# Performance work log

Measured on AMD Instinct MI355X. Metric: run time of the kernel, lower is better.

## Reference

```python
import jax, jax.numpy as jnp
import numpy as np

VOCAB = 32000
EMB = 1024
HID = 1024
CHUNK = 64
NCH = HID // CHUNK          # 16 master-gate chunks
G = 4 * HID + 2 * NCH       # 4128 gate width
T, B = 256, 64


def setup_inputs() -> dict:
    key = jax.random.key(0)
    ks = jax.random.split(key, 8)
    s = 0.02
    return {
        "tokens": jax.random.randint(ks[0], (T, B), 0, VOCAB),
        "emb": jax.random.normal(ks[1], (VOCAB, EMB), jnp.float32) * s,
        "W_ih0": jax.random.normal(ks[2], (EMB, G), jnp.float32) * s,
        "b_ih0": jnp.zeros((G,), jnp.float32),
        "W_hh0": jax.random.normal(ks[3], (HID, G), jnp.float32) * s,
        "b_hh0": jnp.zeros((G,), jnp.float32),
        "W_ih1": jax.random.normal(ks[4], (HID, G), jnp.float32) * s,
        "b_ih1": jnp.zeros((G,), jnp.float32),
        "W_hh1": jax.random.normal(ks[5], (HID, G), jnp.float32) * s,
        "b_hh1": jnp.zeros((G,), jnp.float32),
    }


def _cumsoftmax(x):
    # cumulative softmax along last dim (ordered-neuron master gate)
    return jnp.cumsum(jax.nn.softmax(x, axis=-1), axis=-1)


def _onlstm_layer(x, W_ih, b_ih, W_hh, b_hh):
    # x: (T, B, in_dim) -> (T, B, HID)
    t_in = jnp.einsum('tbi,ig->tbg', x, W_ih) + b_ih  # precomputed ih, as in torch code
    bsz = x.shape[1]
    h0 = jnp.zeros((bsz, HID), x.dtype)
    c0 = jnp.zeros((bsz, NCH, CHUNK), x.dtype)

    def step(carry, tin):
        hx, cx = carry
        gates = tin + hx @ W_hh + b_hh                      # (B, G)
        cingate = 1.0 - _cumsoftmax(gates[:, :NCH])         # (B, NCH)
        cforgetgate = _cumsoftmax(gates[:, NCH:2 * NCH])    # (B, NCH)
        rest = gates[:, 2 * NCH:].reshape(bsz, 4 * NCH, CHUNK)
        outgate, cell, ingate, forgetgate = jnp.split(rest, 4, axis=1)
        outgate = jax.nn.sigmoid(outgate)
        ingate = jax.nn.sigmoid(ingate)
        forgetgate = jax.nn.sigmoid(forgetgate)
        cell = jnp.tanh(cell)
        cing = cingate[:, :, None]
        cfg = cforgetgate[:, :, None]
        overlap = cfg * cing
        fgate = forgetgate * overlap + (cfg - overlap)
        igate = ingate * overlap + (cing - overlap)
        cy = fgate * cx + igate * cell                      # (B, NCH, CHUNK)
        hy = (outgate * jnp.tanh(cy)).reshape(bsz, HID)
        return (hy, cy), hy

    _, hs = jax.lax.scan(step, (h0, c0), t_in)
    return hs


def reference(tokens, emb, W_ih0, b_ih0, W_hh0, b_hh0, W_ih1, b_ih1, W_hh1, b_hh1):
    x = emb[tokens]                                         # (T, B, EMB)
    h1 = _onlstm_layer(x, W_ih0, b_ih0, W_hh0, b_hh0)
    h2 = _onlstm_layer(h1, W_ih1, b_ih1, W_hh1, b_hh1)
    mask = tokens != 0                                      # (T, B)
    return h2, mask
```

## Files before the change

### kernel.cpp

```cpp
#include <hip/hip_runtime.h>

typedef __attribute__((ext_vector_type(8))) short short8;
typedef __attribute__((ext_vector_type(4))) float f32x4;
typedef __attribute__((ext_vector_type(4))) int int4v;
typedef __attribute__((ext_vector_type(4))) unsigned short u16x4;
typedef unsigned short u16;

#define T_LEN 256
#define BATCH 64
#define HID   1024
#define GDIM  4128
#define BH    65536
#define NWG   256

__device__ __forceinline__ u16 f2bf(float f){
  unsigned u = __builtin_bit_cast(unsigned, f);
  return (u16)((u + 0x7fffu + ((u >> 16) & 1u)) >> 16);
}


__global__ __launch_bounds__(1024) void repackW(const float* __restrict__ Wih,
                                                const float* __restrict__ Whh,
                                                u16* __restrict__ Wt)
{
  __shared__ float tile[32][33];
  int k = blockIdx.x * 32 + threadIdx.y;
  int c = blockIdx.y * 32 + threadIdx.x;
  float v = (k < 1024) ? Wih[(size_t)k * GDIM + c]
                       : Whh[(size_t)(k - 1024) * GDIM + c];
  tile[threadIdx.y][threadIdx.x] = v;
  __syncthreads();
  int c2 = blockIdx.y * 32 + threadIdx.y;
  int k2 = blockIdx.x * 32 + threadIdx.x;
  Wt[(size_t)c2 * 2048 + k2] = f2bf(tile[threadIdx.x][threadIdx.y]);
}

__global__ __launch_bounds__(256) void gatherX(const int* __restrict__ tokens,
                                               const float* __restrict__ emb,
                                               u16* __restrict__ x,
                                               float* __restrict__ maskout)
{
  int idx = blockIdx.x;
  int tok = tokens[idx];
  const f32x4* src = (const f32x4*)&emb[(size_t)tok * HID];
  f32x4 v = src[threadIdx.x];
  u16x4 o;
  #pragma unroll
  for (int j = 0; j < 4; ++j) o[j] = f2bf(v[j]);
  *(u16x4*)&x[(size_t)idx * HID + threadIdx.x * 4] = o;
  if (threadIdx.x == 0) maskout[idx] = (tok != 0) ? 1.0f : 0.0f;
}

__global__ __launch_bounds__(256) void biasK(const float* __restrict__ bih0, const float* __restrict__ bhh0,
                                             const float* __restrict__ bih1, const float* __restrict__ bhh1,
                                             float* __restrict__ bias0, float* __restrict__ bias1)
{
  int i = blockIdx.x * 256 + threadIdx.x;
  if (i < GDIM){ bias0[i] = bih0[i] + bhh0[i]; bias1[i] = bih1[i] + bhh1[i]; }
}

__global__ __launch_bounds__(512, 1) void persist(
    const u16* __restrict__ Wt0, const u16* __restrict__ Wt1,
    const float* __restrict__ bias0, const float* __restrict__ bias1,
    const u16* __restrict__ x, u16* __restrict__ hA, u16* __restrict__ hB,
    float* __restrict__ out, unsigned* __restrict__ slots,
    unsigned* __restrict__ flag)
{
  __shared__ __align__(16) u16 Ws[32 * 2048];
  __shared__ __align__(16) float smT[32 * 68];
  __shared__ __align__(16) float restT[32 * 68];

  const int wg = blockIdx.x, tid = threadIdx.x;
  const int lane = tid & 63, wave = tid >> 6;
  const int lo = lane & 15, hi = lane >> 4, khi = hi * 8;
  const int mt = wave >> 1, nw = wave & 1;
  const int row = mt * 16 + lo;
  const int lay = wg >> 7;
  const int E0 = (wg & 127) * 8;
  const u16* Wt = lay ? Wt1 : Wt0;
  const float* bias = lay ? bias1 : bias0;

  auto gcol = [&](int c){ return 32 + (c >> 3) * 1024 + E0 + (c & 7); };

  for (int i = tid; i < 32 * 256; i += 512){
    int c = i >> 8, ck = (i & 255) << 3;
    *(int4v*)&Ws[c * 2048 + (ck ^ ((c & 7) << 3))] =
        *(const int4v*)&Wt[(size_t)gcol(c) * 2048 + ck];
  }

  float bv0, bv1;
  const u16 *gB0 = nullptr, *gB1 = nullptr;
  if (nw == 0){
    bv0 = bias[lo]; bv1 = bias[16 + lo];
    gB0 = Wt + (size_t)lo * 2048;
    gB1 = Wt + (size_t)(16 + lo) * 2048;
  } else {
    bv0 = bias[gcol(lo)]; bv1 = bias[gcol(16 + lo)];
  }
  __syncthreads();

  auto ldsB = [&](int c, int k)->short8 {
    return *(const short8*)&Ws[c * 2048 + (k ^ ((c & 7) << 3))];
  };

  f32x4 xn0, xn1;
  auto slack_mm = [&](const u16* Asrc){
    f32x4 s0 = {bv0,bv0,bv0,bv0}, s1 = {bv1,bv1,bv1,bv1};
    const u16* pA = Asrc + (size_t)row * HID;
    if (nw == 0){
      #pragma unroll 1
      for (int blk = 0; blk < 4; ++blk){
        short8 A[8], B0[8], B1[8];
        #pragma unroll
        for (int i = 0; i < 8; ++i){
          int k = (blk * 8 + i) * 32 + khi;
          A[i]  = *(const short8*)(pA + k);
          B0[i] = *(const short8*)(gB0 + k);
          B1[i] = *(const short8*)(gB1 + k);
        }
        #pragma unroll
        for (int i = 0; i < 8; ++i){
          s0 = __builtin_amdgcn_mfma_f32_16x16x32_bf16(A[i], B0[i], s0, 0,0,0);
          s1 = __builtin_amdgcn_mfma_f32_16x16x32_bf16(A[i], B1[i], s1, 0,0,0);
        }
      }
    } else {
      #pragma unroll 1
      for (int blk = 0; blk < 4; ++blk){
        short8 A[8];
        #pragma unroll
        for (int i = 0; i < 8; ++i)
          A[i] = *(const short8*)(pA + (blk * 8 + i) * 32 + khi);
        #pragma unroll
        for (int i = 0; i < 8; ++i){
          int k = (blk * 8 + i) * 32 + khi;
          s0 = __builtin_amdgcn_mfma_f32_16x16x32_bf16(A[i], ldsB(lo, k), s0, 0,0,0);
          s1 = __builtin_amdgcn_mfma_f32_16x16x32_bf16(A[i], ldsB(16 + lo, k), s1, 0,0,0);
        }
      }
    }
    xn0 = s0; xn1 = s1;
  };

  float creg = 0.f;
  if (lay == 0) slack_mm(x);

  for (int s = 0; s <= 257; ++s){
    const int t = lay ? (s - 2) : s;
    const bool act = (t >= 0) && (t < T_LEN);
    if (act){
      f32x4 a0 = xn0, a1 = xn1;
      if (t > 0){
        const u16* Asrc = lay ? (hB + (size_t)(t - 1) * BH)
                              : (hA + (size_t)(s - 1) * BH);
        const u16* pA = Asrc + (size_t)row * HID;
        if (nw == 0){
          #pragma unroll 1
          for (int blk = 0; blk < 4; ++blk){
            short8 A[8], B0[8], B1[8];
            #pragma unroll
            for (int i = 0; i < 8; ++i){
              int k = (blk * 8 + i) * 32 + khi;
              A[i]  = *(const short8*)(pA + k);
              B0[i] = *(const short8*)(gB0 + 1024 + k);
              B1[i] = *(const short8*)(gB1 + 1024 + k);
            }
            #pragma unroll
            for (int i = 0; i < 8; ++i){
              a0 = __builtin_amdgcn_mfma_f32_16x16x32_bf16(A[i], B0[i], a0, 0,0,0);
              a1 = __builtin_amdgcn_mfma_f32_16x16x32_bf16(A[i], B1[i], a1, 0,0,0);
            }
          }
        } else {
          #pragma unroll 1
          for (int blk = 0; blk < 4; ++blk){
            short8 A[8];
            #pragma unroll
            for (int i = 0; i < 8; ++i)
              A[i] = *(const short8*)(pA + (blk * 8 + i) * 32 + khi);
            #pragma unroll
            for (int i = 0; i < 8; ++i){
              int k = 1024 + (blk * 8 + i) * 32 + khi;
              a0 = __builtin_amdgcn_mfma_f32_16x16x32_bf16(A[i], ldsB(lo, k), a0, 0,0,0);
              a1 = __builtin_amdgcn_mfma_f32_16x16x32_bf16(A[i], ldsB(16 + lo, k), a1, 0,0,0);
            }
          }
        }
      }
      const int r0 = mt * 16 + hi * 4;
      if (nw == 0){
        *(f32x4*)&smT[lo * 68 + r0] = a0;
        *(f32x4*)&smT[(16 + lo) * 68 + r0] = a1;
      } else {
        *(f32x4*)&restT[lo * 68 + r0] = a0;
        *(f32x4*)&restT[(16 + lo) * 68 + r0] = a1;
      }
      __syncthreads();
      {
        const int r = tid >> 3, j = tid & 7;
        const int n = (wg & 127) >> 3;
        float m1 = -1e30f, m2 = -1e30f;
        float l1[16], l2[16];
        #pragma unroll
        for (int i = 0; i < 16; ++i){
          l1[i] = smT[i * 68 + r]; l2[i] = smT[(16 + i) * 68 + r];
          m1 = fmaxf(m1, l1[i]);   m2 = fmaxf(m2, l2[i]);
        }
        float s1 = 0.f, s2 = 0.f, cu1 = 0.f, cu2 = 0.f;
        #pragma unroll
        for (int i = 0; i < 16; ++i){
          float e1 = __expf(l1[i] - m1), e2 = __expf(l2[i] - m2);
          s1 += e1; s2 += e2;
          if (i <= n){ cu1 += e1; cu2 += e2; }
        }
        const float cin = 1.f - cu1 / s1;
        const float cf  = cu2 / s2;
        const float ov  = cf * cin;
        const float og = restT[j * 68 + r];
        const float ce = restT[(8 + j) * 68 + r];
        const float ig = restT[(16 + j) * 68 + r];
        const float fg = restT[(24 + j) * 68 + r];
        const float ogv = 1.f / (1.f + __expf(-og));
        const float inv = 1.f / (1.f + __expf(-ig));
        const float fgv = 1.f / (1.f + __expf(-fg));
        const float cev = tanhf(ce);
        if (t == 0) creg = 0.f;
        const float fga = fgv * ov + (cf - ov);
        const float iga = inv * ov + (cin - ov);
        const float cy  = fga * creg + iga * cev;
        creg = cy;
        const float hy = ogv * tanhf(cy);
        const u16 hb = f2bf(hy);
        if (lay == 0){
          *(volatile u16*)&hA[(size_t)t * BH + r * HID + E0 + j] = hb;
        } else {
          out[((size_t)t * BATCH + r) * HID + E0 + j] = hy;
          *(volatile u16*)&hB[(size_t)t * BH + r * HID + E0 + j] = hb;
        }
      }
    }
    asm volatile("s_waitcnt vmcnt(0)" ::: "memory");
    __syncthreads();
    if (tid == 0) *(volatile unsigned*)&slots[wg * 32] = (unsigned)(s + 1);
    if (lay == 0){
      if (s <= T_LEN - 2) slack_mm(x + (size_t)(s + 1) * BH);
    } else {
      if (s >= 1 && s <= T_LEN) slack_mm(hA + (size_t)(s - 1) * BH);
    }
    const unsigned tg = (unsigned)(s + 1);
    if (wg == 0){
      if (wave == 0){
        for (;;){
          int ok = 1;
          #pragma unroll
          for (int q = 0; q < 4; ++q)
            ok &= (*(volatile const unsigned*)&slots[(lane + q * 64) * 32] >= tg);
          if (__all(ok)) break;
          __builtin_amdgcn_s_sleep(2);
        }
        if (lane == 0) *(volatile unsigned*)flag = tg;
      }
    } else {
      if (tid == 0)
        while (*(volatile const unsigned*)flag < tg) __builtin_amdgcn_s_sleep(4);
    }
    __syncthreads();
  }
}


extern "C" void kernel_launch(void* const* d_in, const int* in_sizes, int n_in,
                              void* d_out, int out_size, void* d_ws, size_t ws_size,
                              hipStream_t stream)
{
  (void)in_sizes; (void)n_in; (void)out_size; (void)ws_size;
  const int*   tokens = (const int*)d_in[0];
  const float* emb    = (const float*)d_in[1];
  const float* Wih0   = (const float*)d_in[2];
  const float* bih0   = (const float*)d_in[3];
  const float* Whh0   = (const float*)d_in[4];
  const float* bhh0   = (const float*)d_in[5];
  const float* Wih1   = (const float*)d_in[6];
  const float* bih1   = (const float*)d_in[7];
  const float* Whh1   = (const float*)d_in[8];
  const float* bhh1   = (const float*)d_in[9];
  float* out = (float*)d_out;

  char* ws = (char*)d_ws;
  u16*   Wt0    = (u16*)(ws);
  u16*   Wt1    = (u16*)(ws + 16908288);
  u16*   x      = (u16*)(ws + 33816576);
  u16*   hA     = (u16*)(ws + 67371008);
  u16*   hB     = (u16*)(ws + 100925440);
  float* bias0  = (float*)(ws + 134479872);
  float* bias1  = (float*)(ws + 134496384);
  unsigned* slots = (unsigned*)(ws + 134512896);
  unsigned* flag  = (unsigned*)(ws + 134545664);

  repackW<<<dim3(64,129), dim3(32,32), 0, stream>>>(Wih0, Whh0, Wt0);
  repackW<<<dim3(64,129), dim3(32,32), 0, stream>>>(Wih1, Whh1, Wt1);
  gatherX<<<16384, 256, 0, stream>>>(tokens, emb, x, out + 16777216);
  biasK<<<17, 256, 0, stream>>>(bih0, bhh0, bih1, bhh1, bias0, bias1);
  hipMemsetAsync(slots, 0, 33024, stream);

  persist<<<NWG, 512, 0, stream>>>(Wt0, Wt1, bias0, bias1, x, hA, hB,
                                   out, slots, flag);
}
```

Baseline: 8.190 ms.

## Replace master-flag barrier with distributed slot polling and stage h stores via LDS

The grid barrier changes from a two-level scheme (WG0 polls all slots, then publishes a flag that the other workgroups poll) to one where every workgroup polls a packed slot array directly with vector loads and no sleep. Slots are now packed densely instead of padded to 128 bytes. Hidden-state and output writes are staged in LDS and written as 16-byte vector stores instead of scalar 2-byte and 4-byte stores. The A operand is preloaded fully (32 registers) ahead of the MFMA loops. These aim to cut barrier latency and store traffic on the serial recurrence, at the cost of more polling contention, possible false sharing on the slots, and higher register pressure.

```diff
diff --git a/kernel.cpp b/kernel.cpp
--- a/kernel.cpp
+++ b/kernel.cpp
@@ -63,12 +63,13 @@
     const u16* __restrict__ Wt0, const u16* __restrict__ Wt1,
     const float* __restrict__ bias0, const float* __restrict__ bias1,
     const u16* __restrict__ x, u16* __restrict__ hA, u16* __restrict__ hB,
-    float* __restrict__ out, unsigned* __restrict__ slots,
-    unsigned* __restrict__ flag)
+    float* __restrict__ out, unsigned* __restrict__ slots)
 {
   __shared__ __align__(16) u16 Ws[32 * 2048];
   __shared__ __align__(16) float smT[32 * 68];
   __shared__ __align__(16) float restT[32 * 68];
+  __shared__ __align__(16) u16 hStage[64 * 8];
+  __shared__ __align__(16) float oStage[64 * 8];
 
   const int wg = blockIdx.x, tid = threadIdx.x;
   const int lane = tid & 63, wave = tid >> 6;
@@ -103,47 +104,44 @@
     return *(const short8*)&Ws[c * 2048 + (k ^ ((c & 7) << 3))];
   };
 
-  f32x4 xn0, xn1;
-  auto slack_mm = [&](const u16* Asrc){
-    f32x4 s0 = {bv0,bv0,bv0,bv0}, s1 = {bv1,bv1,bv1,bv1};
+  auto mm = [&](const u16* Asrc, int koff, f32x4& r0, f32x4& r1){
     const u16* pA = Asrc + (size_t)row * HID;
+    short8 A[32];
+    #pragma unroll
+    for (int i = 0; i < 32; ++i) A[i] = *(const short8*)(pA + i * 32 + khi);
     if (nw == 0){
       #pragma unroll 1
       for (int blk = 0; blk < 4; ++blk){
-        short8 A[8], B0[8], B1[8];
+        short8 B0[8], B1[8];
         #pragma unroll
         for (int i = 0; i < 8; ++i){
-          int k = (blk * 8 + i) * 32 + khi;
-          A[i]  = *(const short8*)(pA + k);
+          int k = koff + (blk * 8 + i) * 32 + khi;
           B0[i] = *(const short8*)(gB0 + k);
           B1[i] = *(const short8*)(gB1 + k);
         }
         #pragma unroll
         for (int i = 0; i < 8; ++i){
-          s0 = __builtin_amdgcn_mfma_f32_16x16x32_bf16(A[i], B0[i], s0, 0,0,0);
-          s1 = __builtin_amdgcn_mfma_f32_16x16x32_bf16(A[i], B1[i], s1, 0,0,0);
+          r0 = __builtin_amdgcn_mfma_f32_16x16x32_bf16(A[blk * 8 + i], B0[i], r0, 0,0,0);
+          r1 = __builtin_amdgcn_mfma_f32_16x16x32_bf16(A[blk * 8 + i], B1[i], r1, 0,0,0);
         }
       }
     } else {
       #pragma unroll 1
       for (int blk = 0; blk < 4; ++blk){
-        short8 A[8];
-        #pragma unroll
-        for (int i = 0; i < 8; ++i)
-          A[i] = *(const short8*)(pA + (blk * 8 + i) * 32 + khi);
         #pragma unroll
         for (int i = 0; i < 8; ++i){
-          int k = (blk * 8 + i) * 32 + khi;
-          s0 = __builtin_amdgcn_mfma_f32_16x16x32_bf16(A[i], ldsB(lo, k), s0, 0,0,0);
-          s1 = __builtin_amdgcn_mfma_f32_16x16x32_bf16(A[i], ldsB(16 + lo, k), s1, 0,0,0);
-        }
-      }
-    }
-    xn0 = s0; xn1 = s1;
+          int k = koff + (blk * 8 + i) * 32 + khi;
+          r0 = __builtin_amdgcn_mfma_f32_16x16x32_bf16(A[blk * 8 + i], ldsB(lo, k), r0, 0,0,0);
+          r1 = __builtin_amdgcn_mfma_f32_16x16x32_bf16(A[blk * 8 + i], ldsB(16 + lo, k), r1, 0,0,0);
+        }
+      }
+    }
   };
 
+  f32x4 xn0, xn1;
   float creg = 0.f;
-  if (lay == 0) slack_mm(x);
+  if (lay == 0){ xn0 = f32x4{bv0,bv0,bv0,bv0}; xn1 = f32x4{bv1,bv1,bv1,bv1};
+                 mm(x, 0, xn0, xn1); }
 
   for (int s = 0; s <= 257; ++s){
     const int t = lay ? (s - 2) : s;
@@ -153,47 +151,15 @@
       if (t > 0){
         const u16* Asrc = lay ? (hB + (size_t)(t - 1) * BH)
                               : (hA + (size_t)(s - 1) * BH);
-        const u16* pA = Asrc + (size_t)row * HID;
-        if (nw == 0){
-          #pragma unroll 1
-          for (int blk = 0; blk < 4; ++blk){
-            short8 A[8], B0[8], B1[8];
-            #pragma unroll
-            for (int i = 0; i < 8; ++i){
-              int k = (blk * 8 + i) * 32 + khi;
-              A[i]  = *(const short8*)(pA + k);
-              B0[i] = *(const short8*)(gB0 + 1024 + k);
-              B1[i] = *(const short8*)(gB1 + 1024 + k);
-            }
-            #pragma unroll
-            for (int i = 0; i < 8; ++i){
-              a0 = __builtin_amdgcn_mfma_f32_16x16x32_bf16(A[i], B0[i], a0, 0,0,0);
-              a1 = __builtin_amdgcn_mfma_f32_16x16x32_bf16(A[i], B1[i], a1, 0,0,0);
-            }
-          }
-        } else {
-          #pragma unroll 1
-          for (int blk = 0; blk < 4; ++blk){
-            short8 A[8];
-            #pragma unroll
-            for (int i = 0; i < 8; ++i)
-              A[i] = *(const short8*)(pA + (blk * 8 + i) * 32 + khi);
-            #pragma unroll
-            for (int i = 0; i < 8; ++i){
-              int k = 1024 + (blk * 8 + i) * 32 + khi;
-              a0 = __builtin_amdgcn_mfma_f32_16x16x32_bf16(A[i], ldsB(lo, k), a0, 0,0,0);
-              a1 = __builtin_amdgcn_mfma_f32_16x16x32_bf16(A[i], ldsB(16 + lo, k), a1, 0,0,0);
-            }
-          }
-        }
-      }
-      const int r0 = mt * 16 + hi * 4;
+        mm(Asrc, 1024, a0, a1);
+      }
+      const int r0i = mt * 16 + hi * 4;
       if (nw == 0){
-        *(f32x4*)&smT[lo * 68 + r0] = a0;
-        *(f32x4*)&smT[(16 + lo) * 68 + r0] = a1;
+        *(f32x4*)&smT[lo * 68 + r0i] = a0;
+        *(f32x4*)&smT[(16 + lo) * 68 + r0i] = a1;
       } else {
-        *(f32x4*)&restT[lo * 68 + r0] = a0;
-        *(f32x4*)&restT[(16 + lo) * 68 + r0] = a1;
+        *(f32x4*)&restT[lo * 68 + r0i] = a0;
+        *(f32x4*)&restT[(16 + lo) * 68 + r0i] = a1;
       }
       __syncthreads();
       {
@@ -230,41 +196,48 @@
         const float cy  = fga * creg + iga * cev;
         creg = cy;
         const float hy = ogv * tanhf(cy);
-        const u16 hb = f2bf(hy);
-        if (lay == 0){
-          *(volatile u16*)&hA[(size_t)t * BH + r * HID + E0 + j] = hb;
-        } else {
-          out[((size_t)t * BATCH + r) * HID + E0 + j] = hy;
-          *(volatile u16*)&hB[(size_t)t * BH + r * HID + E0 + j] = hb;
-        }
+        hStage[r * 8 + j] = f2bf(hy);
+        if (lay) oStage[r * 8 + j] = hy;
+      }
+      __syncthreads();
+      if (tid < 64){
+        int4v hv = *(const int4v*)&hStage[tid * 8];
+        u16* dst = (lay ? hB : hA) + (size_t)t * BH + tid * HID + E0;
+        *(volatile int4v*)dst = hv;
+      } else if (lay && tid < 192){
+        int w = tid - 64;
+        int r = w >> 1, half = w & 1;
+        f32x4 ov4 = *(const f32x4*)&oStage[r * 8 + half * 4];
+        *(f32x4*)&out[((size_t)t * BATCH + r) * HID + E0 + half * 4] = ov4;
       }
     }
     asm volatile("s_waitcnt vmcnt(0)" ::: "memory");
     __syncthreads();
-    if (tid == 0) *(volatile unsigned*)&slots[wg * 32] = (unsigned)(s + 1);
+    if (tid == 0) *(volatile unsigned*)&slots[wg] = (unsigned)(s + 1);
     if (lay == 0){
-      if (s <= T_LEN - 2) slack_mm(x + (size_t)(s + 1) * BH);
+      if (s <= T_LEN - 2){
+        xn0 = f32x4{bv0,bv0,bv0,bv0}; xn1 = f32x4{bv1,bv1,bv1,bv1};
+        mm(x + (size_t)(s + 1) * BH, 0, xn0, xn1);
+      }
     } else {
-      if (s >= 1 && s <= T_LEN) slack_mm(hA + (size_t)(s - 1) * BH);
-    }
-    const unsigned tg = (unsigned)(s + 1);
-    if (wg == 0){
-      if (wave == 0){
+      if (s >= 1 && s <= T_LEN){
+        xn0 = f32x4{bv0,bv0,bv0,bv0}; xn1 = f32x4{bv1,bv1,bv1,bv1};
+        mm(hA + (size_t)(s - 1) * BH, 0, xn0, xn1);
+      }
+    }
+    if (s < 257){
+      const unsigned tg = (unsigned)(s + 1);
+      if (tid < 64){
+        const volatile int4v* sp = (const volatile int4v*)&slots[tid * 4];
         for (;;){
-          int ok = 1;
-          #pragma unroll
-          for (int q = 0; q < 4; ++q)
-            ok &= (*(volatile const unsigned*)&slots[(lane + q * 64) * 32] >= tg);
+          int4v v = *sp;
+          int ok = ((unsigned)v[0] >= tg) & ((unsigned)v[1] >= tg) &
+                   ((unsigned)v[2] >= tg) & ((unsigned)v[3] >= tg);
           if (__all(ok)) break;
-          __builtin_amdgcn_s_sleep(2);
-        }
-        if (lane == 0) *(volatile unsigned*)flag = tg;
-      }
-    } else {
-      if (tid == 0)
-        while (*(volatile const unsigned*)flag < tg) __builtin_amdgcn_s_sleep(4);
-    }
-    __syncthreads();
+        }
+      }
+      __syncthreads();
+    }
   }
 }
 
@@ -295,14 +268,13 @@
   float* bias0  = (float*)(ws + 134479872);
   float* bias1  = (float*)(ws + 134496384);
   unsigned* slots = (unsigned*)(ws + 134512896);
-  unsigned* flag  = (unsigned*)(ws + 134545664);
 
   repackW<<<dim3(64,129), dim3(32,32), 0, stream>>>(Wih0, Whh0, Wt0);
   repackW<<<dim3(64,129), dim3(32,32), 0, stream>>>(Wih1, Whh1, Wt1);
   gatherX<<<16384, 256, 0, stream>>>(tokens, emb, x, out + 16777216);
   biasK<<<17, 256, 0, stream>>>(bih0, bhh0, bih1, bhh1, bias0, bias1);
-  hipMemsetAsync(slots, 0, 33024, stream);
+  hipMemsetAsync(slots, 0, 1024, stream);
 
   persist<<<NWG, 512, 0, stream>>>(Wt0, Wt1, bias0, bias1, x, hA, hB,
-                                   out, slots, flag);
-}
+                                   out, slots);
+}
```

Measured after the change: 15.73 ms. 1.92x slower.

## Replace centralized flag barrier with distributed packed-slot polling and staged stores

Applied to the files above, without the earlier changes.

The two-level barrier, where workgroup 0 polls padded slots and then publishes a flag, is replaced by every workgroup polling a packed array of 256 slot counters directly, using vectorized 16-byte loads and no sleep. The per-thread scattered bf16 hidden-state and fp32 output stores are first staged in LDS and then written as 16-byte vector stores by a subset of threads. Each workgroup now signals its slot right after its own h store completes, not after a full-block wait, which shortens the critical path of the per-step grid barrier. The trade-off is more polling traffic on a shared cache line from all workgroups, plus an extra __syncthreads for the staging step.

```diff
diff --git a/kernel.cpp b/kernel.cpp
--- a/kernel.cpp
+++ b/kernel.cpp
@@ -63,12 +63,13 @@
     const u16* __restrict__ Wt0, const u16* __restrict__ Wt1,
     const float* __restrict__ bias0, const float* __restrict__ bias1,
     const u16* __restrict__ x, u16* __restrict__ hA, u16* __restrict__ hB,
-    float* __restrict__ out, unsigned* __restrict__ slots,
-    unsigned* __restrict__ flag)
+    float* __restrict__ out, unsigned* __restrict__ slots)
 {
   __shared__ __align__(16) u16 Ws[32 * 2048];
   __shared__ __align__(16) float smT[32 * 68];
   __shared__ __align__(16) float restT[32 * 68];
+  __shared__ __align__(16) u16 hStage[64 * 8];
+  __shared__ __align__(16) float oStage[64 * 8];
 
   const int wg = blockIdx.x, tid = threadIdx.x;
   const int lane = tid & 63, wave = tid >> 6;
@@ -180,20 +181,20 @@
               A[i] = *(const short8*)(pA + (blk * 8 + i) * 32 + khi);
             #pragma unroll
             for (int i = 0; i < 8; ++i){
-              int k = 1024 + (blk * 8 + i) * 32 + khi;
-              a0 = __builtin_amdgcn_mfma_f32_16x16x32_bf16(A[i], ldsB(lo, k), a0, 0,0,0);
-              a1 = __builtin_amdgcn_mfma_f32_16x16x32_bf16(A[i], ldsB(16 + lo, k), a1, 0,0,0);
+              int k = (blk * 8 + i) * 32 + khi;
+              a0 = __builtin_amdgcn_mfma_f32_16x16x32_bf16(A[i], ldsB(lo, 1024 + k), a0, 0,0,0);
+              a1 = __builtin_amdgcn_mfma_f32_16x16x32_bf16(A[i], ldsB(16 + lo, 1024 + k), a1, 0,0,0);
             }
           }
         }
       }
-      const int r0 = mt * 16 + hi * 4;
+      const int r0i = mt * 16 + hi * 4;
       if (nw == 0){
-        *(f32x4*)&smT[lo * 68 + r0] = a0;
-        *(f32x4*)&smT[(16 + lo) * 68 + r0] = a1;
+        *(f32x4*)&smT[lo * 68 + r0i] = a0;
+        *(f32x4*)&smT[(16 + lo) * 68 + r0i] = a1;
       } else {
-        *(f32x4*)&restT[lo * 68 + r0] = a0;
-        *(f32x4*)&restT[(16 + lo) * 68 + r0] = a1;
+        *(f32x4*)&restT[lo * 68 + r0i] = a0;
+        *(f32x4*)&restT[(16 + lo) * 68 + r0i] = a1;
       }
       __syncthreads();
       {
@@ -230,41 +231,43 @@
         const float cy  = fga * creg + iga * cev;
         creg = cy;
         const float hy = ogv * tanhf(cy);
-        const u16 hb = f2bf(hy);
-        if (lay == 0){
-          *(volatile u16*)&hA[(size_t)t * BH + r * HID + E0 + j] = hb;
-        } else {
-          out[((size_t)t * BATCH + r) * HID + E0 + j] = hy;
-          *(volatile u16*)&hB[(size_t)t * BH + r * HID + E0 + j] = hb;
-        }
-      }
+        hStage[r * 8 + j] = f2bf(hy);
+        if (lay) oStage[r * 8 + j] = hy;
+      }
+      __syncthreads();
+      if (tid < 64){
+        int4v hv = *(const int4v*)&hStage[tid * 8];
+        u16* dst = (lay ? hB : hA) + (size_t)t * BH + tid * HID + E0;
+        *(volatile int4v*)dst = hv;
+        asm volatile("s_waitcnt vmcnt(0)" ::: "memory");
+        if (tid == 0) *(volatile unsigned*)&slots[wg] = (unsigned)(s + 1);
+      } else if (lay && tid < 192){
+        int w = tid - 64;
+        int r = w >> 1, half = w & 1;
+        f32x4 ov4 = *(const f32x4*)&oStage[r * 8 + half * 4];
+        *(f32x4*)&out[((size_t)t * BATCH + r) * HID + E0 + half * 4] = ov4;
+      }
+    } else {
+      if (tid == 0) *(volatile unsigned*)&slots[wg] = (unsigned)(s + 1);
     }
-    asm volatile("s_waitcnt vmcnt(0)" ::: "memory");
-    __syncthreads();
-    if (tid == 0) *(volatile unsigned*)&slots[wg * 32] = (unsigned)(s + 1);
     if (lay == 0){
       if (s <= T_LEN - 2) slack_mm(x + (size_t)(s + 1) * BH);
     } else {
       if (s >= 1 && s <= T_LEN) slack_mm(hA + (size_t)(s - 1) * BH);
     }
-    const unsigned tg = (unsigned)(s + 1);
-    if (wg == 0){
-      if (wave == 0){
+    if (s < 257){
+      const unsigned tg = (unsigned)(s + 1);
+      if (tid < 64){
+        const volatile int4v* sp = (const volatile int4v*)&slots[tid * 4];
         for (;;){
-          int ok = 1;
-          #pragma unroll
-          for (int q = 0; q < 4; ++q)
-            ok &= (*(volatile const unsigned*)&slots[(lane + q * 64) * 32] >= tg);
+          int4v v = *sp;
+          int ok = ((unsigned)v[0] >= tg) & ((unsigned)v[1] >= tg) &
+                   ((unsigned)v[2] >= tg) & ((unsigned)v[3] >= tg);
           if (__all(ok)) break;
-          __builtin_amdgcn_s_sleep(2);
-        }
-        if (lane == 0) *(volatile unsigned*)flag = tg;
-      }
-    } else {
-      if (tid == 0)
-        while (*(volatile const unsigned*)flag < tg) __builtin_amdgcn_s_sleep(4);
+        }
+      }
+      __syncthreads();
     }
-    __syncthreads();
   }
 }
 
@@ -295,14 +298,13 @@
   float* bias0  = (float*)(ws + 134479872);
   float* bias1  = (float*)(ws + 134496384);
   unsigned* slots = (unsigned*)(ws + 134512896);
-  unsigned* flag  = (unsigned*)(ws + 134545664);
 
   repackW<<<dim3(64,129), dim3(32,32), 0, stream>>>(Wih0, Whh0, Wt0);
   repackW<<<dim3(64,129), dim3(32,32), 0, stream>>>(Wih1, Whh1, Wt1);
   gatherX<<<16384, 256, 0, stream>>>(tokens, emb, x, out + 16777216);
   biasK<<<17, 256, 0, stream>>>(bih0, bhh0, bih1, bhh1, bias0, bias1);
-  hipMemsetAsync(slots, 0, 33024, stream);
+  hipMemsetAsync(slots, 0, 1024, stream);
 
   persist<<<NWG, 512, 0, stream>>>(Wt0, Wt1, bias0, bias1, x, hA, hB,
-                                   out, slots, flag);
-}
+                                   out, slots);
+}
```

After: 7.796 ms. 1.05x faster.
